# Performance work log

Measured on AMD Instinct MI355X. Metric: run time of the kernel, lower is better.

Reference implementation:

```python
import jax, jax.numpy as jnp
import numpy as np

N = 100000  # nodes
E = 1600000  # edges
F_IN = 512
H = 128
C = 40
L = 8
ALPHA = 0.1
THETA = 0.5


def setup_inputs() -> dict:
    key = jax.random.key(0)
    ks = jax.random.split(key, 8)
    x = jax.random.normal(ks[0], (N, F_IN), dtype=jnp.float32)
    edge_index = jax.random.randint(ks[1], (2, E), 0, N, dtype=jnp.int32)
    edge_weight = jax.random.uniform(ks[2], (E,), dtype=jnp.float32)
    W0 = jax.random.normal(ks[3], (F_IN, H), dtype=jnp.float32) * 0.05
    b0 = jnp.zeros((H,), dtype=jnp.float32)
    convW = jax.random.normal(ks[4], (L, H, H), dtype=jnp.float32) * 0.05
    W1 = jax.random.normal(ks[5], (H, C), dtype=jnp.float32) * 0.05
    b1 = jnp.zeros((C,), dtype=jnp.float32)
    return {"x": x, "edge_index": edge_index, "edge_weight": edge_weight,
            "W0": W0, "b0": b0, "convW": convW, "W1": W1, "b1": b1}


def reference(x, edge_index, edge_weight, W0, b0, convW, W1, b1):
    # eval mode, dropout=0.0 -> dropout is identity
    src, dst = edge_index[0], edge_index[1]
    h = jnp.maximum(x @ W0 + b0, 0.0)  # [N, H]
    x0 = h  # initial residual
    # GCN2Conv beta per layer: log(theta/layer + 1), layer = 1..L
    betas = jnp.log(THETA / jnp.arange(1, L + 1, dtype=jnp.float32) + 1.0)

    def layer(h, inputs):
        W, beta = inputs  # W: [H, H]
        # sparse adjacency propagation: sum_j A_ij * h_j
        msgs = h[src] * edge_weight[:, None]  # [E, H]
        agg = jax.ops.segment_sum(msgs, dst, num_segments=N)  # [N, H]
        # initial residual mixing + identity mapping (shared_weights=True)
        out = (1.0 - ALPHA) * agg + ALPHA * x0
        out = (1.0 - beta) * out + beta * (out @ W)
        return jnp.maximum(out, 0.0), None

    h, _ = jax.lax.scan(layer, h, (convW, betas))
    logits = h @ W1 + b1  # [N, C]
    return jax.nn.log_softmax(logits, axis=-1)
```

## Files before the change

### kernel.cpp

```cpp
#include <hip/hip_runtime.h>
#include <hip/hip_bf16.h>
#include <cmath>

#define NN 100000
#define NE 1600000
#define FIN 512
#define HD 128
#define NC 40
#define NL 8
#define NBK 196
#define P1B 256
#define CHUNK ((NE + P1B - 1) / P1B)

typedef __attribute__((ext_vector_type(8))) short bh8;
typedef __attribute__((ext_vector_type(4))) float f4;
typedef __attribute__((ext_vector_type(4))) unsigned int u4;
typedef __attribute__((ext_vector_type(2))) unsigned int u2;

__device__ __forceinline__ float bflo(unsigned p){ return __uint_as_float(p << 16); }
__device__ __forceinline__ float bfhi(unsigned p){ return __uint_as_float(p & 0xffff0000u); }
__device__ __forceinline__ unsigned short f2bf(float f){
  unsigned u = __float_as_uint(f);
  u += 0x7fffu + ((u >> 16) & 1u);
  return (unsigned short)(u >> 16);
}
__device__ __forceinline__ unsigned pack2(float a, float b){
  return (unsigned)f2bf(a) | ((unsigned)f2bf(b) << 16);
}

__global__ __launch_bounds__(256) void k_hist(const int* __restrict__ dst,
                                              int* __restrict__ bcnt){
  __shared__ int h[256];
  int t = threadIdx.x;
  h[t] = 0;
  __syncthreads();
  int lo = blockIdx.x * CHUNK;
  int hi = lo + CHUNK < NE ? lo + CHUNK : NE;
  for (int i = lo + t; i < hi; i += 256)
    atomicAdd(&h[dst[i] >> 9], 1);
  __syncthreads();
  if (h[t]) atomicAdd(&bcnt[t], h[t]);
}

__global__ void k_bscan(const int* __restrict__ bcnt, int* __restrict__ gbase,
                        int* __restrict__ gcur, int* __restrict__ offs){
  int t = threadIdx.x;
  int carry = 0;
  for (int base = 0; base < 256; base += 64){
    int v = bcnt[base + t];
    int orig = v;
    #pragma unroll
    for (int off = 1; off < 64; off <<= 1){
      int u = __shfl_up(v, off);
      if (t >= off) v += u;
    }
    int excl = carry + v - orig;
    gbase[base + t] = excl;
    gcur[base + t] = excl;
    carry += __shfl(v, 63);
  }
  if (t == 0){ gbase[256] = carry; offs[NN] = NE; }
}

__global__ __launch_bounds__(256) void k_part(const int* __restrict__ src,
                                              const int* __restrict__ dst,
                                              const float* __restrict__ w,
                                              int* __restrict__ gcur,
                                              u2* __restrict__ tmp){
  __shared__ int h[256];
  __shared__ int base[256];
  int t = threadIdx.x;
  h[t] = 0;
  __syncthreads();
  int lo = blockIdx.x * CHUNK;
  int hi = lo + CHUNK < NE ? lo + CHUNK : NE;
  for (int i = lo + t; i < hi; i += 256)
    atomicAdd(&h[dst[i] >> 9], 1);
  __syncthreads();
  int cnt = h[t];
  if (cnt) base[t] = atomicAdd(&gcur[t], cnt);
  h[t] = 0;
  __syncthreads();
  for (int i = lo + t; i < hi; i += 256){
    int d = dst[i];
    int bk = d >> 9;
    int r = atomicAdd(&h[bk], 1);
    u2 v = { (unsigned)src[i] | ((unsigned)(d & 511) << 17), __float_as_uint(w[i]) };
    tmp[base[bk] + r] = v;
  }
}

__global__ __launch_bounds__(256) void k_place(const u2* __restrict__ tmp,
                                               const int* __restrict__ gbase,
                                               int* __restrict__ offs,
                                               u2* __restrict__ epk){
  __shared__ int h[512];
  __shared__ int lofs[512];
  int b = blockIdx.x;
  int t = threadIdx.x;
  int e0 = gbase[b], e1 = gbase[b + 1];
  h[t] = 0; h[t + 256] = 0;
  __syncthreads();
  for (int i = e0 + t; i < e1; i += 256)
    atomicAdd(&h[tmp[i].x >> 17], 1);
  __syncthreads();
  if (t < 64){
    int carry = 0;
    for (int base = 0; base < 512; base += 64){
      int v = h[base + t];
      int orig = v;
      #pragma unroll
      for (int off = 1; off < 64; off <<= 1){
        int u = __shfl_up(v, off);
        if (t >= off) v += u;
      }
      lofs[base + t] = carry + v - orig;
      carry += __shfl(v, 63);
    }
  }
  __syncthreads();
  int d = b * 512 + t;
  if (d < NN) offs[d] = e0 + lofs[t];
  int d2 = b * 512 + 256 + t;
  if (d2 < NN) offs[d2] = e0 + lofs[256 + t];
  h[t] = 0; h[t + 256] = 0;
  __syncthreads();
  for (int i = e0 + t; i < e1; i += 256){
    u2 v = tmp[i];
    int d9 = v.x >> 17;
    int r = atomicAdd(&h[d9], 1);
    u2 o = { v.x & 0x1FFFFu, v.y };
    epk[e0 + lofs[d9] + r] = o;
  }
}

__global__ void k_twt_all(const float* __restrict__ W0, const float* __restrict__ cW,
                          const float* __restrict__ W1, unsigned short* __restrict__ out){
  const int n0 = FIN * HD;
  const int n1 = NL * HD * HD;
  const int total = n0 + n1 + 48 * HD;
  for (int i = blockIdx.x * blockDim.x + threadIdx.x; i < total; i += gridDim.x * blockDim.x){
    float v;
    if (i < n0){
      int c = i / FIN, k = i % FIN;
      v = W0[(size_t)k * HD + c];
    } else if (i < n0 + n1){
      int j = i - n0;
      int l = j / (HD * HD), r = j % (HD * HD);
      int c = r / HD, k = r % HD;
      v = cW[(size_t)l * HD * HD + k * HD + c];
    } else {
      int j = i - n0 - n1;
      int c = j / HD, k = j % HD;
      v = (c < NC) ? W1[(size_t)k * NC + c] : 0.f;
    }
    out[i] = f2bf(v);
  }
}

__global__ __launch_bounds__(256) void k_gemm0(const float* __restrict__ X,
                                               const unsigned short* __restrict__ Wt,
                                               const float* __restrict__ b0,
                                               unsigned* __restrict__ Ha,
                                               unsigned* __restrict__ Hb, int n){
  __shared__ __attribute__((aligned(16))) char lds[33792];
  char* ldsA = lds;
  char* ldsW = lds + 8192;
  float* ldsO = (float*)lds;
  int t = threadIdx.x;
  int w = t >> 6, lane = t & 63;
  int rowBase = blockIdx.x * 64;
  f4 acc[8];
  #pragma unroll
  for (int i = 0; i < 8; i++) acc[i] = (f4)0.f;

  for (int kk = 0; kk < 8; kk++){
    #pragma unroll
    for (int iter = 0; iter < 2; iter++){
      int r = t / 8 + iter * 32;
      int kc = (t % 8) * 8;
      int grow = rowBase + r;
      float4 f0 = {0,0,0,0}, f1 = {0,0,0,0};
      if (grow < n){
        const float4* p = (const float4*)(X + (size_t)grow * FIN + kk * 64 + kc);
        f0 = p[0]; f1 = p[1];
      }
      u4 pv = { pack2(f0.x, f0.y), pack2(f0.z, f0.w), pack2(f1.x, f1.y), pack2(f1.z, f1.w) };
      *(u4*)(ldsA + r * 128 + ((kc * 2) ^ ((r & 7) << 4))) = pv;
    }
    #pragma unroll
    for (int iter = 0; iter < 4; iter++){
      int c = t / 8 + iter * 32;
      int kc = (t % 8) * 8;
      bh8 v = *(const bh8*)(Wt + (size_t)c * FIN + kk * 64 + kc);
      *(bh8*)(ldsW + c * 128 + ((kc * 2) ^ ((c & 7) << 4))) = v;
    }
    __syncthreads();
    int rowf = (w << 4) + (lane & 15);
    #pragma unroll
    for (int ks = 0; ks < 2; ks++){
      bh8 fa = *(const bh8*)(ldsA + rowf * 128 + ((ks * 64 + (lane >> 4) * 16) ^ ((rowf & 7) << 4)));
      #pragma unroll
      for (int ct = 0; ct < 8; ct++){
        int colf = (ct << 4) + (lane & 15);
        bh8 fb = *(const bh8*)(ldsW + colf * 128 + ((ks * 64 + (lane >> 4) * 16) ^ ((colf & 7) << 4)));
        acc[ct] = __builtin_amdgcn_mfma_f32_16x16x32_bf16(fa, fb, acc[ct], 0, 0, 0);
      }
    }
    __syncthreads();
  }
  #pragma unroll
  for (int ct = 0; ct < 8; ct++){
    int colf = (ct << 4) + (lane & 15);
    float bb = b0[colf];
    #pragma unroll
    for (int i = 0; i < 4; i++){
      int r = (w << 4) + ((lane >> 4) << 2) + i;
      float v = acc[ct][i] + bb;
      ldsO[r * 132 + colf] = v > 0.f ? v : 0.f;
    }
  }
  __syncthreads();
  #pragma unroll
  for (int iter = 0; iter < 4; iter++){
    int r = iter * 16 + t / 16;
    int c8 = (t % 16) * 8;
    int grow = rowBase + r;
    if (grow < n){
      float* p = &ldsO[r * 132 + c8];
      u4 pv = { pack2(p[0], p[1]), pack2(p[2], p[3]), pack2(p[4], p[5]), pack2(p[6], p[7]) };
      *(u4*)(Ha + (size_t)grow * 64 + (t % 16) * 4) = pv;
      *(u4*)(Hb + (size_t)grow * 64 + (t % 16) * 4) = pv;
    }
  }
}

__global__ __launch_bounds__(512) void k_layer(const unsigned* __restrict__ Hin,
                                               const unsigned* __restrict__ X0,
                                               const int* __restrict__ offs,
                                               const u2* __restrict__ epk,
                                               const unsigned short* __restrict__ Wt,
                                               float beta,
                                               unsigned* __restrict__ Hout, int n){
  __shared__ __attribute__((aligned(16))) char ldsA[16384];
  int t = threadIdx.x;
  int w = t >> 6, lane = t & 63;
  int q = lane >> 4, l16 = lane & 15;
  int quadId = (w << 2) + q;
  int rowBase = blockIdx.x * 64;

  #pragma unroll
  for (int rr = 0; rr < 2; rr++){
    int lr = (quadId << 1) + rr;
    int d = rowBase + lr;
    bool act = d < n;
    int e0 = act ? offs[d] : 0;
    int e1 = act ? offs[d + 1] : 0;
    float a0=0.f,a1=0.f,a2=0.f,a3=0.f,a4=0.f,a5=0.f,a6=0.f,a7=0.f;
    int e = e0;
    for (; e + 7 < e1; e += 8){
      #pragma unroll
      for (int j = 0; j < 8; j++){
        u2 pe = epk[e + j];
        float wf = __uint_as_float(pe.y);
        u4 r = *(const u4*)(Hin + (size_t)pe.x * 64 + l16 * 4);
        a0 += wf * bflo(r.x); a1 += wf * bfhi(r.x);
        a2 += wf * bflo(r.y); a3 += wf * bfhi(r.y);
        a4 += wf * bflo(r.z); a5 += wf * bfhi(r.z);
        a6 += wf * bflo(r.w); a7 += wf * bfhi(r.w);
      }
    }
    for (; e < e1; e++){
      u2 pe = epk[e];
      float wf = __uint_as_float(pe.y);
      u4 r = *(const u4*)(Hin + (size_t)pe.x * 64 + l16 * 4);
      a0 += wf * bflo(r.x); a1 += wf * bfhi(r.x);
      a2 += wf * bflo(r.y); a3 += wf * bfhi(r.y);
      a4 += wf * bflo(r.z); a5 += wf * bfhi(r.z);
      a6 += wf * bflo(r.w); a7 += wf * bfhi(r.w);
    }
    u4 ov = { 0u, 0u, 0u, 0u };
    if (act){
      u4 xp = *(const u4*)(X0 + (size_t)d * 64 + l16 * 4);
      float v0 = 0.9f*a0 + 0.1f*bflo(xp.x), v1 = 0.9f*a1 + 0.1f*bfhi(xp.x);
      float v2 = 0.9f*a2 + 0.1f*bflo(xp.y), v3 = 0.9f*a3 + 0.1f*bfhi(xp.y);
      float v4 = 0.9f*a4 + 0.1f*bflo(xp.z), v5 = 0.9f*a5 + 0.1f*bfhi(xp.z);
      float v6 = 0.9f*a6 + 0.1f*bflo(xp.w), v7 = 0.9f*a7 + 0.1f*bfhi(xp.w);
      ov = (u4){ pack2(v0,v1), pack2(v2,v3), pack2(v4,v5), pack2(v6,v7) };
    }
    *(u4*)(ldsA + lr * 256 + ((l16 * 16) ^ ((lr & 7) << 4))) = ov;
  }
  __syncthreads();

  f4 acc[4];
  #pragma unroll
  for (int i = 0; i < 4; i++) acc[i] = (f4)0.f;
  int rowf = ((w & 3) << 4) + l16;
  int colBase = (w >> 2) << 6;
  #pragma unroll
  for (int ks = 0; ks < 4; ks++){
    bh8 fa = *(const bh8*)(ldsA + rowf * 256 + ((ks * 64 + q * 16) ^ ((rowf & 7) << 4)));
    #pragma unroll
    for (int ct = 0; ct < 4; ct++){
      int colf = colBase + (ct << 4) + l16;
      bh8 fb = *(const bh8*)(Wt + (size_t)colf * HD + ks * 32 + q * 8);
      acc[ct] = __builtin_amdgcn_mfma_f32_16x16x32_bf16(fa, fb, acc[ct], 0, 0, 0);
    }
  }

  #pragma unroll
  for (int ct = 0; ct < 4; ct++){
    int colf = colBase + (ct << 4) + l16;
    #pragma unroll
    for (int i = 0; i < 4; i++){
      int r = ((w & 3) << 4) + (q << 2) + i;
      char* addr = ldsA + r * 256 + ((colf * 2) ^ ((r & 7) << 4));
      unsigned short tv = *(const unsigned short*)addr;
      float tf = __uint_as_float(((unsigned)tv) << 16);
      float v = (1.f - beta) * tf + beta * acc[ct][i];
      *(unsigned short*)addr = f2bf(v > 0.f ? v : 0.f);
    }
  }
  __syncthreads();

  #pragma unroll
  for (int iter = 0; iter < 2; iter++){
    int r = iter * 32 + t / 16;
    int kc = (t % 16) * 8;
    int grow = rowBase + r;
    if (grow < n){
      bh8 v = *(const bh8*)(ldsA + r * 256 + ((kc * 2) ^ ((r & 7) << 4)));
      *(bh8*)((unsigned short*)Hout + (size_t)grow * HD + kc) = v;
    }
  }
}

__global__ __launch_bounds__(256) void k_final(const unsigned* __restrict__ H,
                                               const unsigned short* __restrict__ W1t,
                                               const float* __restrict__ b1,
                                               float* __restrict__ out, int n){
  __shared__ __attribute__((aligned(16))) char lds[16384 + 12288];
  char* ldsA = lds;
  char* ldsW = lds + 16384;
  int t = threadIdx.x;
  int w = t >> 6, lane = t & 63;
  int l15 = lane & 15;
  int rowBase = blockIdx.x * 64;
  const unsigned short* Hs = (const unsigned short*)H;

  #pragma unroll
  for (int iter = 0; iter < 4; iter++){
    int r = t / 16 + iter * 16;
    int kc = (t % 16) * 8;
    int grow = rowBase + r;
    bh8 v = (bh8)(short)0;
    if (grow < n) v = *(const bh8*)(Hs + (size_t)grow * HD + kc);
    *(bh8*)(ldsA + r * 256 + ((kc * 2) ^ ((r & 7) << 4))) = v;
  }
  #pragma unroll
  for (int iter = 0; iter < 3; iter++){
    int c = t / 16 + iter * 16;
    int kc = (t % 16) * 8;
    bh8 v = *(const bh8*)(W1t + (size_t)c * HD + kc);
    *(bh8*)(ldsW + c * 256 + ((kc * 2) ^ ((c & 7) << 4))) = v;
  }
  __syncthreads();

  f4 acc[3];
  #pragma unroll
  for (int i = 0; i < 3; i++) acc[i] = (f4)0.f;
  int rowf = (w << 4) + l15;
  #pragma unroll
  for (int ks = 0; ks < 4; ks++){
    bh8 fa = *(const bh8*)(ldsA + rowf * 256 + ((ks * 64 + (lane >> 4) * 16) ^ ((rowf & 7) << 4)));
    #pragma unroll
    for (int ct = 0; ct < 3; ct++){
      int colf = (ct << 4) + l15;
      bh8 fb = *(const bh8*)(ldsW + colf * 256 + ((ks * 64 + (lane >> 4) * 16) ^ ((colf & 7) << 4)));
      acc[ct] = __builtin_amdgcn_mfma_f32_16x16x32_bf16(fa, fb, acc[ct], 0, 0, 0);
    }
  }

  float bias0 = b1[l15];
  float bias1 = b1[16 + l15];
  bool v2ok = (l15 < 8);
  float bias2 = v2ok ? b1[32 + l15] : 0.f;

  #pragma unroll
  for (int i = 0; i < 4; i++){
    int r = rowBase + (w << 4) + ((lane >> 4) << 2) + i;
    float v0 = acc[0][i] + bias0;
    float v1 = acc[1][i] + bias1;
    float v2 = v2ok ? (acc[2][i] + bias2) : -1e30f;
    float m = fmaxf(fmaxf(v0, v1), v2);
    #pragma unroll
    for (int off = 1; off < 16; off <<= 1) m = fmaxf(m, __shfl_xor(m, off));
    float e0 = __expf(v0 - m), e1 = __expf(v1 - m);
    float e2 = v2ok ? __expf(v2 - m) : 0.f;
    float s = e0 + e1 + e2;
    #pragma unroll
    for (int off = 1; off < 16; off <<= 1) s += __shfl_xor(s, off);
    float ls = m + __logf(s);
    if (r < n){
      out[(size_t)r * NC + l15] = v0 - ls;
      out[(size_t)r * NC + 16 + l15] = v1 - ls;
      if (v2ok) out[(size_t)r * NC + 32 + l15] = v2 - ls;
    }
  }
}

extern "C" void kernel_launch(void* const* d_in, const int* in_sizes, int n_in,
                              void* d_out, int out_size, void* d_ws, size_t ws_size,
                              hipStream_t stream){
  const float* x  = (const float*)d_in[0];
  const int*   ei = (const int*)d_in[1];
  const float* ew = (const float*)d_in[2];
  const float* W0 = (const float*)d_in[3];
  const float* b0 = (const float*)d_in[4];
  const float* cW = (const float*)d_in[5];
  const float* W1 = (const float*)d_in[6];
  const float* b1 = (const float*)d_in[7];
  float* out = (float*)d_out;
  const int* src = ei;
  const int* dst = ei + NE;

  char* ws = (char*)d_ws;
  size_t off = 0;
  auto alloc = [&](size_t bytes) -> char* {
    char* p = ws + off;
    off += (bytes + 255) & ~(size_t)255;
    return p;
  };
  unsigned* x0b = (unsigned*)alloc((size_t)NN * 64 * 4);
  unsigned* hbA = (unsigned*)alloc((size_t)NN * 64 * 4);
  unsigned* hbB = (unsigned*)alloc((size_t)NN * 64 * 4);
  unsigned short* wbuf = (unsigned short*)alloc(((size_t)FIN * HD + (size_t)NL * HD * HD + 48 * HD) * 2);
  unsigned short* W0t = wbuf;
  unsigned short* cWt = wbuf + (size_t)FIN * HD;
  unsigned short* W1t = cWt + (size_t)NL * HD * HD;
  int*   offs  = (int*)alloc((size_t)(NN + 1) * 4);
  int*   bcnt  = (int*)alloc(256 * 4);
  int*   gbase = (int*)alloc(257 * 4);
  int*   gcur  = (int*)alloc(256 * 4);
  u2*    tmp   = (u2*)alloc((size_t)NE * 8);
  u2*    epk   = (u2*)alloc((size_t)NE * 8);

  (void)hipMemsetAsync(bcnt, 0, 256 * 4, stream);
  hipLaunchKernelGGL(k_hist, dim3(P1B), dim3(256), 0, stream, dst, bcnt);
  hipLaunchKernelGGL(k_bscan, dim3(1), dim3(64), 0, stream, bcnt, gbase, gcur, offs);
  hipLaunchKernelGGL(k_part, dim3(P1B), dim3(256), 0, stream, src, dst, ew, gcur, tmp);
  hipLaunchKernelGGL(k_place, dim3(NBK), dim3(256), 0, stream, tmp, gbase, offs, epk);
  hipLaunchKernelGGL(k_twt_all, dim3(256), dim3(256), 0, stream, W0, cW, W1, wbuf);

  int gblocks = (NN + 63) / 64;
  hipLaunchKernelGGL(k_gemm0, dim3(gblocks), dim3(256), 0, stream, x, W0t, b0, x0b, hbA, NN);
  for (int l = 0; l < NL; l++){
    float beta = logf(0.5f / (float)(l + 1) + 1.0f);
    const unsigned* hin = (l & 1) ? hbB : hbA;
    unsigned* hout = (l & 1) ? hbA : hbB;
    hipLaunchKernelGGL(k_layer, dim3(gblocks), dim3(512), 0, stream,
                       hin, x0b, offs, epk, cWt + (size_t)l * HD * HD, beta, hout, NN);
  }
  hipLaunchKernelGGL(k_final, dim3(gblocks), dim3(256), 0, stream, hbA, W1t, b1, out, NN);
}
```

Baseline: 1.000 ms.

## Make layer kernel persistent with atomic tile scheduler and predicated edge loop

Each layer kernel now launches a fixed grid of 1024 blocks that pull 64-row tiles from a per-layer global atomic counter until none remain, replacing one block per tile. The edge loop becomes a single predicated 8-wide unrolled loop with no scalar tail, where lanes past the end gather row 0 with zero weight. The aim is to cut block launch overhead and balance tiles of uneven degree. In exchange it adds an atomic and extra barriers per tile, plus wasted gathers on padded edges.

```diff
diff --git a/kernel.cpp b/kernel.cpp
--- a/kernel.cpp
+++ b/kernel.cpp
@@ -11,6 +11,8 @@
 #define NBK 196
 #define P1B 256
 #define CHUNK ((NE + P1B - 1) / P1B)
+#define NTILES ((NN + 63) / 64)
+#define LGRID 1024
 
 typedef __attribute__((ext_vector_type(8))) short bh8;
 typedef __attribute__((ext_vector_type(4))) float f4;
@@ -241,97 +243,99 @@
                                                const u2* __restrict__ epk,
                                                const unsigned short* __restrict__ Wt,
                                                float beta,
-                                               unsigned* __restrict__ Hout, int n){
+                                               unsigned* __restrict__ Hout, int n,
+                                               int* __restrict__ ctr){
   __shared__ __attribute__((aligned(16))) char ldsA[16384];
+  __shared__ int sTile;
   int t = threadIdx.x;
   int w = t >> 6, lane = t & 63;
   int q = lane >> 4, l16 = lane & 15;
   int quadId = (w << 2) + q;
-  int rowBase = blockIdx.x * 64;
-
-  #pragma unroll
-  for (int rr = 0; rr < 2; rr++){
-    int lr = (quadId << 1) + rr;
-    int d = rowBase + lr;
-    bool act = d < n;
-    int e0 = act ? offs[d] : 0;
-    int e1 = act ? offs[d + 1] : 0;
-    float a0=0.f,a1=0.f,a2=0.f,a3=0.f,a4=0.f,a5=0.f,a6=0.f,a7=0.f;
-    int e = e0;
-    for (; e + 7 < e1; e += 8){
+
+  for (;;){
+    if (t == 0) sTile = atomicAdd(ctr, 1);
+    __syncthreads();
+    int tile = sTile;
+    if (tile >= NTILES) break;
+    int rowBase = tile * 64;
+
+    #pragma unroll
+    for (int rr = 0; rr < 2; rr++){
+      int lr = (quadId << 1) + rr;
+      int d = rowBase + lr;
+      bool act = d < n;
+      int e0 = act ? offs[d] : 0;
+      int e1 = act ? offs[d + 1] : 0;
+      float a0=0.f,a1=0.f,a2=0.f,a3=0.f,a4=0.f,a5=0.f,a6=0.f,a7=0.f;
+      for (int e = e0; e < e1; e += 8){
+        #pragma unroll
+        for (int j = 0; j < 8; j++){
+          int ee = e + j;
+          u2 pe = { 0u, 0u };
+          if (ee < e1) pe = epk[ee];
+          float wf = __uint_as_float(pe.y);
+          u4 r = *(const u4*)(Hin + (size_t)pe.x * 64 + l16 * 4);
+          a0 += wf * bflo(r.x); a1 += wf * bfhi(r.x);
+          a2 += wf * bflo(r.y); a3 += wf * bfhi(r.y);
+          a4 += wf * bflo(r.z); a5 += wf * bfhi(r.z);
+          a6 += wf * bflo(r.w); a7 += wf * bfhi(r.w);
+        }
+      }
+      u4 ov = { 0u, 0u, 0u, 0u };
+      if (act){
+        u4 xp = *(const u4*)(X0 + (size_t)d * 64 + l16 * 4);
+        float v0 = 0.9f*a0 + 0.1f*bflo(xp.x), v1 = 0.9f*a1 + 0.1f*bfhi(xp.x);
+        float v2 = 0.9f*a2 + 0.1f*bflo(xp.y), v3 = 0.9f*a3 + 0.1f*bfhi(xp.y);
+        float v4 = 0.9f*a4 + 0.1f*bflo(xp.z), v5 = 0.9f*a5 + 0.1f*bfhi(xp.z);
+        float v6 = 0.9f*a6 + 0.1f*bflo(xp.w), v7 = 0.9f*a7 + 0.1f*bfhi(xp.w);
+        ov = (u4){ pack2(v0,v1), pack2(v2,v3), pack2(v4,v5), pack2(v6,v7) };
+      }
+      *(u4*)(ldsA + lr * 256 + ((l16 * 16) ^ ((lr & 7) << 4))) = ov;
+    }
+    __syncthreads();
+
+    f4 acc[4];
+    #pragma unroll
+    for (int i = 0; i < 4; i++) acc[i] = (f4)0.f;
+    int rowf = ((w & 3) << 4) + l16;
+    int colBase = (w >> 2) << 6;
+    #pragma unroll
+    for (int ks = 0; ks < 4; ks++){
+      bh8 fa = *(const bh8*)(ldsA + rowf * 256 + ((ks * 64 + q * 16) ^ ((rowf & 7) << 4)));
       #pragma unroll
-      for (int j = 0; j < 8; j++){
-        u2 pe = epk[e + j];
-        float wf = __uint_as_float(pe.y);
-        u4 r = *(const u4*)(Hin + (size_t)pe.x * 64 + l16 * 4);
-        a0 += wf * bflo(r.x); a1 += wf * bfhi(r.x);
-        a2 += wf * bflo(r.y); a3 += wf * bfhi(r.y);
-        a4 += wf * bflo(r.z); a5 += wf * bfhi(r.z);
-        a6 += wf * bflo(r.w); a7 += wf * bfhi(r.w);
-      }
-    }
-    for (; e < e1; e++){
-      u2 pe = epk[e];
-      float wf = __uint_as_float(pe.y);
-      u4 r = *(const u4*)(Hin + (size_t)pe.x * 64 + l16 * 4);
-      a0 += wf * bflo(r.x); a1 += wf * bfhi(r.x);
-      a2 += wf * bflo(r.y); a3 += wf * bfhi(r.y);
-      a4 += wf * bflo(r.z); a5 += wf * bfhi(r.z);
-      a6 += wf * bflo(r.w); a7 += wf * bfhi(r.w);
-    }
-    u4 ov = { 0u, 0u, 0u, 0u };
-    if (act){
-      u4 xp = *(const u4*)(X0 + (size_t)d * 64 + l16 * 4);
-      float v0 = 0.9f*a0 + 0.1f*bflo(xp.x), v1 = 0.9f*a1 + 0.1f*bfhi(xp.x);
-      float v2 = 0.9f*a2 + 0.1f*bflo(xp.y), v3 = 0.9f*a3 + 0.1f*bfhi(xp.y);
-      float v4 = 0.9f*a4 + 0.1f*bflo(xp.z), v5 = 0.9f*a5 + 0.1f*bfhi(xp.z);
-      float v6 = 0.9f*a6 + 0.1f*bflo(xp.w), v7 = 0.9f*a7 + 0.1f*bfhi(xp.w);
-      ov = (u4){ pack2(v0,v1), pack2(v2,v3), pack2(v4,v5), pack2(v6,v7) };
-    }
-    *(u4*)(ldsA + lr * 256 + ((l16 * 16) ^ ((lr & 7) << 4))) = ov;
-  }
-  __syncthreads();
-
-  f4 acc[4];
-  #pragma unroll
-  for (int i = 0; i < 4; i++) acc[i] = (f4)0.f;
-  int rowf = ((w & 3) << 4) + l16;
-  int colBase = (w >> 2) << 6;
-  #pragma unroll
-  for (int ks = 0; ks < 4; ks++){
-    bh8 fa = *(const bh8*)(ldsA + rowf * 256 + ((ks * 64 + q * 16) ^ ((rowf & 7) << 4)));
+      for (int ct = 0; ct < 4; ct++){
+        int colf = colBase + (ct << 4) + l16;
+        bh8 fb = *(const bh8*)(Wt + (size_t)colf * HD + ks * 32 + q * 8);
+        acc[ct] = __builtin_amdgcn_mfma_f32_16x16x32_bf16(fa, fb, acc[ct], 0, 0, 0);
+      }
+    }
+
     #pragma unroll
     for (int ct = 0; ct < 4; ct++){
       int colf = colBase + (ct << 4) + l16;
-      bh8 fb = *(const bh8*)(Wt + (size_t)colf * HD + ks * 32 + q * 8);
-      acc[ct] = __builtin_amdgcn_mfma_f32_16x16x32_bf16(fa, fb, acc[ct], 0, 0, 0);
-    }
-  }
-
-  #pragma unroll
-  for (int ct = 0; ct < 4; ct++){
-    int colf = colBase + (ct << 4) + l16;
-    #pragma unroll
-    for (int i = 0; i < 4; i++){
-      int r = ((w & 3) << 4) + (q << 2) + i;
-      char* addr = ldsA + r * 256 + ((colf * 2) ^ ((r & 7) << 4));
-      unsigned short tv = *(const unsigned short*)addr;
-      float tf = __uint_as_float(((unsigned)tv) << 16);
-      float v = (1.f - beta) * tf + beta * acc[ct][i];
-      *(unsigned short*)addr = f2bf(v > 0.f ? v : 0.f);
-    }
-  }
-  __syncthreads();
-
-  #pragma unroll
-  for (int iter = 0; iter < 2; iter++){
-    int r = iter * 32 + t / 16;
-    int kc = (t % 16) * 8;
-    int grow = rowBase + r;
-    if (grow < n){
-      bh8 v = *(const bh8*)(ldsA + r * 256 + ((kc * 2) ^ ((r & 7) << 4)));
-      *(bh8*)((unsigned short*)Hout + (size_t)grow * HD + kc) = v;
-    }
+      #pragma unroll
+      for (int i = 0; i < 4; i++){
+        int r = ((w & 3) << 4) + (q << 2) + i;
+        char* addr = ldsA + r * 256 + ((colf * 2) ^ ((r & 7) << 4));
+        unsigned short tv = *(const unsigned short*)addr;
+        float tf = __uint_as_float(((unsigned)tv) << 16);
+        float v = (1.f - beta) * tf + beta * acc[ct][i];
+        *(unsigned short*)addr = f2bf(v > 0.f ? v : 0.f);
+      }
+    }
+    __syncthreads();
+
+    #pragma unroll
+    for (int iter = 0; iter < 2; iter++){
+      int r = iter * 32 + t / 16;
+      int kc = (t % 16) * 8;
+      int grow = rowBase + r;
+      if (grow < n){
+        bh8 v = *(const bh8*)(ldsA + r * 256 + ((kc * 2) ^ ((r & 7) << 4)));
+        *(bh8*)((unsigned short*)Hout + (size_t)grow * HD + kc) = v;
+      }
+    }
+    __syncthreads();
   }
 }
 
@@ -442,10 +446,12 @@
   int*   bcnt  = (int*)alloc(256 * 4);
   int*   gbase = (int*)alloc(257 * 4);
   int*   gcur  = (int*)alloc(256 * 4);
+  int*   ctrs  = (int*)alloc(NL * 4);
   u2*    tmp   = (u2*)alloc((size_t)NE * 8);
   u2*    epk   = (u2*)alloc((size_t)NE * 8);
 
   (void)hipMemsetAsync(bcnt, 0, 256 * 4, stream);
+  (void)hipMemsetAsync(ctrs, 0, NL * 4, stream);
   hipLaunchKernelGGL(k_hist, dim3(P1B), dim3(256), 0, stream, dst, bcnt);
   hipLaunchKernelGGL(k_bscan, dim3(1), dim3(64), 0, stream, bcnt, gbase, gcur, offs);
   hipLaunchKernelGGL(k_part, dim3(P1B), dim3(256), 0, stream, src, dst, ew, gcur, tmp);
@@ -458,8 +464,9 @@
     float beta = logf(0.5f / (float)(l + 1) + 1.0f);
     const unsigned* hin = (l & 1) ? hbB : hbA;
     unsigned* hout = (l & 1) ? hbA : hbB;
-    hipLaunchKernelGGL(k_layer, dim3(gblocks), dim3(512), 0, stream,
-                       hin, x0b, offs, epk, cWt + (size_t)l * HD * HD, beta, hout, NN);
+    hipLaunchKernelGGL(k_layer, dim3(LGRID), dim3(512), 0, stream,
+                       hin, x0b, offs, epk, cWt + (size_t)l * HD * HD, beta, hout, NN,
+                       ctrs + l);
   }
   hipLaunchKernelGGL(k_final, dim3(gblocks), dim3(256), 0, stream, hbA, W1t, b1, out, NN);
 }
```

Measured after the change: 1.071 ms. 1.07x slower.
